# Kernel tuning notes

Measured on AMD Instinct MI355X. Metric: run time of the kernel, lower is better.

## Reference

```python
import jax, jax.numpy as jnp
import numpy as np

B, N, E, H, L, T, IN = 32, 512, 32768, 64, 2, 2, 8
TAU = 0.5


def setup_inputs() -> dict:
    key = jax.random.key(0)
    ks = jax.random.split(key, 32)
    f = lambda i, shape, s=0.05: jax.random.normal(ks[i], shape, jnp.float32) * s
    u = jax.random.uniform(ks[3], (B, E, T), jnp.float32, 1e-6, 1.0 - 1e-6)
    return {
        "inputs": f(0, (B, N, IN), 1.0),
        "hidden": f(1, (B, N, H), 1.0),
        "edge_logits": f(2, (B, E, T), 1.0),
        "gumbel": -jnp.log(-jnp.log(u)),  # standard Gumbel noise (deterministic here)
        "send_edges": jax.random.randint(ks[4], (E,), 0, N),
        "recv_edges": jax.random.randint(ks[5], (E,), 0, N),
        "W1": f(6, (L, T, H, 2 * H)), "b1": f(7, (L, T, H)),
        "W2": f(8, (L, T, H, H)), "b2": f(9, (L, T, H)),
        "Whr": f(10, (H, L * H)), "Whi": f(11, (H, L * H)), "Whh": f(12, (H, L * H)),
        "Wir": f(13, (H, IN)), "bir": f(14, (H,)),
        "Wii": f(15, (H, IN)), "bii": f(16, (H,)),
        "Win": f(17, (H, IN)), "bin_w": f(18, (H,)),
        "Wm1": f(19, (H, H)), "bm1": f(20, (H,)),
        "Wm2": f(21, (H, H)), "bm2": f(22, (H,)),
        "Wdf": f(23, (N, N * H), 0.005), "bdf": f(24, (N,)),
        "Wloc": f(25, (N, N * H), 0.005), "bloc": f(26, (N,)),
        "Wscale": f(27, (N, N * H), 0.005), "bscale": f(28, (N,)),
    }


def _lin(x, W, b):
    return jnp.einsum('...i,oi->...o', x, W) + b


def reference(inputs, hidden, edge_logits, gumbel, send_edges, recv_edges,
              W1, b1, W2, b2, Whr, Whi, Whh,
              Wir, bir, Wii, bii, Win, bin_w,
              Wm1, bm1, Wm2, bm2,
              Wdf, bdf, Wloc, bloc, Wscale, bscale):
    # hard gumbel-softmax (straight-through)
    y_soft = jax.nn.softmax((edge_logits + gumbel) / TAU, axis=-1)
    y_hard = jax.nn.one_hot(jnp.argmax(y_soft, axis=-1), T, dtype=y_soft.dtype)
    edges = jax.lax.stop_gradient(y_hard - y_soft) + y_soft  # [B,E,T]

    # normalized receiver degree (zeros -> 1), as in edge2node_mat / degree
    deg = jnp.zeros((N,), jnp.float32).at[recv_edges].add(1.0)
    deg = jnp.where(deg == 0, 1.0, deg)

    hidden_ = hidden
    aggs = []
    norm = float(T)  # skip_first_edge_type=False
    for k in range(L):
        pre = jnp.concatenate([hidden_[:, recv_edges], hidden_[:, send_edges]], axis=-1)  # [B,E,2H]
        all_msgs = jnp.zeros((B, E, H), pre.dtype)
        for t in range(T):  # per-edge-type tanh MLP (eval mode: dropout off)
            m = jnp.tanh(jnp.einsum('bef,hf->beh', pre, W1[k, t]) + b1[k, t])
            m = jnp.tanh(jnp.einsum('beh,gh->beg', m, W2[k, t]) + b2[k, t])
            all_msgs = all_msgs + m * edges[:, :, t:t + 1] / norm
        # scatter-mean onto receiver nodes (= normalized edge2node matmul)
        agg = jnp.zeros((B, N, H), all_msgs.dtype).at[:, recv_edges].add(all_msgs) / deg[None, :, None]
        hidden_ = agg
        aggs.append(agg)
    agg = jnp.concatenate(aggs, axis=-1)  # [B,N,L*H]

    r = jax.nn.sigmoid(_lin(inputs, Wir, bir) + jnp.einsum('bnf,of->bno', agg, Whr))
    i = jax.nn.sigmoid(_lin(inputs, Wii, bii) + jnp.einsum('bnf,of->bno', agg, Whi))
    n = jnp.tanh(_lin(inputs, Win, bin_w) + r * jnp.einsum('bnf,of->bno', agg, Whh))
    hidden_new = (1.0 - i) * n + i * hidden  # [B,N,H]

    pred = _lin(jax.nn.relu(_lin(hidden_new, Wm1, bm1)), Wm2, bm2)
    flat = pred.reshape(B, -1)  # [B, N*H]
    df = 2.0 + jax.nn.softplus(flat @ Wdf.T + bdf)      # StudentT domain maps
    loc = flat @ Wloc.T + bloc
    scale = jax.nn.softplus(flat @ Wscale.T + bscale)
    return df, loc, scale, hidden_new, edges
```

## Files before the change

### kernel.cpp

```cpp
#include <hip/hip_runtime.h>

#define B_  32
#define N_  512
#define E_  32768
#define H_  64
#define L_  2
#define T_  2
#define IN_ 8

typedef __attribute__((ext_vector_type(4))) float f32x4;
typedef __attribute__((ext_vector_type(8))) short bf16x8;
typedef __attribute__((ext_vector_type(4))) short s16x4;

__device__ __forceinline__ short f2bf(float f){
  unsigned u = __float_as_uint(f);
  u += 0x7FFFu + ((u >> 16) & 1u);
  return (short)(u >> 16);
}
__device__ __forceinline__ float bf2f(short s){
  return __uint_as_float(((unsigned)(unsigned short)s) << 16);
}
__device__ __forceinline__ bf16x8 pack8(f32x4 a, f32x4 b){
  bf16x8 r;
  r[0]=f2bf(a[0]); r[1]=f2bf(a[1]); r[2]=f2bf(a[2]); r[3]=f2bf(a[3]);
  r[4]=f2bf(b[0]); r[5]=f2bf(b[1]); r[6]=f2bf(b[2]); r[7]=f2bf(b[3]);
  return r;
}
__device__ __forceinline__ float fast_tanh(float x){
  float e = __expf(2.0f * x);
  return 1.0f - __fdividef(2.0f, e + 1.0f);
}
__device__ __forceinline__ float fast_sigm(float x){
  return __fdividef(1.0f, 1.0f + __expf(-x));
}
__device__ __forceinline__ float softplus_f(float x){
  return fmaxf(x, 0.0f) + log1pf(__expf(-fabsf(x)));
}

__global__ void k_edges(const float* __restrict__ logits, const float* __restrict__ gum,
                        float* __restrict__ edges_out, unsigned char* __restrict__ type_out){
  int i = blockIdx.x * 256 + threadIdx.x;
  if(i >= B_ * E_) return;
  float l0 = logits[2*i]   + gum[2*i];
  float l1 = logits[2*i+1] + gum[2*i+1];
  int t = (l1 > l0) ? 1 : 0;
  edges_out[2*i]   = t ? 0.f : 1.f;
  edges_out[2*i+1] = t ? 1.f : 0.f;
  type_out[i] = (unsigned char)t;
}

__global__ void k_hist(const int* __restrict__ recvE, int* __restrict__ hist){
  int e = blockIdx.x * 256 + threadIdx.x;
  if(e < E_) atomicAdd(&hist[recvE[e]], 1);
}
__global__ void k_scan(const int* __restrict__ hist, int* __restrict__ row_start,
                       float* __restrict__ deg){
  __shared__ int a[512], bbuf[512];
  int t = threadIdx.x;
  int h = hist[t];
  a[t] = h;
  __syncthreads();
  int* cur = a; int* nxt = bbuf;
  for(int off = 1; off < 512; off <<= 1){
    int v = cur[t] + (t >= off ? cur[t - off] : 0);
    nxt[t] = v;
    __syncthreads();
    int* tmp = cur; cur = nxt; nxt = tmp;
  }
  row_start[t] = cur[t] - h;
  if(t == 0) row_start[512] = E_;
  deg[t] = (h == 0) ? 1.0f : (float)h;
}

__global__ void k_hist2(const int* __restrict__ recvE, const unsigned char* __restrict__ typ,
                        int* __restrict__ n0){
  __shared__ int lh[512];
  int b = blockIdx.y, tid = threadIdx.x;
  lh[tid] = 0; lh[tid + 256] = 0;
  __syncthreads();
  int e0 = blockIdx.x * 2048;
  for(int k = 0; k < 8; ++k){
    int e = e0 + k*256 + tid;
    if(typ[(size_t)b*E_ + e] == 0) atomicAdd(&lh[recvE[e]], 1);
  }
  __syncthreads();
  if(lh[tid])       atomicAdd(&n0[b*512 + tid],       lh[tid]);
  if(lh[tid + 256]) atomicAdd(&n0[b*512 + tid + 256], lh[tid + 256]);
}
__global__ void k_scan2(const int* __restrict__ n0, const int* __restrict__ row_start,
                        int* __restrict__ stt){
  __shared__ int a[512], bbuf[512];
  __shared__ int tot;
  int b = blockIdx.x, t = threadIdx.x;
  int h = n0[b*512 + t];
  a[t] = h;
  __syncthreads();
  int* cur = a; int* nxt = bbuf;
  for(int off = 1; off < 512; off <<= 1){
    int v = cur[t] + (t >= off ? cur[t - off] : 0);
    nxt[t] = v;
    __syncthreads();
    int* tmp = cur; cur = nxt; nxt = tmp;
  }
  if(t == 511) tot = cur[511];
  __syncthreads();
  int excl = cur[t] - h;
  stt[(b*2    )*513 + t] = excl;
  stt[(b*2 + 1)*513 + t] = tot + row_start[t] - excl;
  if(t == 0){ stt[(b*2)*513 + 512] = tot; stt[(b*2+1)*513 + 512] = E_; }
}
__global__ void k_perm2(const int* __restrict__ recvE, const unsigned char* __restrict__ typ,
                        const int* __restrict__ stt, int* __restrict__ cur0,
                        int* __restrict__ cur1, unsigned short* __restrict__ perm2){
  int i = blockIdx.x * 256 + threadIdx.x;
  int b = i >> 15, e = i & (E_ - 1);
  int r = recvE[e];
  int pos;
  if(typ[i] == 0) pos = stt[(b*2  )*513 + r] + atomicAdd(&cur0[b*512 + r], 1);
  else            pos = stt[(b*2+1)*513 + r] + atomicAdd(&cur1[b*512 + r], 1);
  perm2[(size_t)b*E_ + pos] = (unsigned short)e;
}

__launch_bounds__(256, 2)
__global__ void k_prep(const float* __restrict__ hid,
                       const float* __restrict__ W1, const float* __restrict__ b1,
                       unsigned short* __restrict__ P, int layer){
  __shared__ __align__(16) short WT[256 * 64];
  __shared__ float bias[256];
  __shared__ float hidl[32 * 64];

  const int tid = threadIdx.x;
  const int b   = blockIdx.y;
  const int nbase = blockIdx.x * 32;
  const float* W1k = W1 + layer * (T_ * H_ * 2 * H_);

  {
    int col = tid, slot = col >> 6, h = col & 63;
    int t = slot & 1, prt = slot >> 1;
    const float* src = W1k + t*8192 + h*128 + prt*64;
#pragma unroll
    for(int u = 0; u < 8; ++u){
      bf16x8 v = pack8(*(const f32x4*)(src + u*8), *(const f32x4*)(src + u*8 + 4));
      int bo = col*128 + ((u*16) ^ ((col & 7) << 4));
      *(bf16x8*)((char*)WT + bo) = v;
    }
    bias[col] = (slot < 2) ? b1[layer*128 + t*64 + h] : 0.0f;
  }
  {
    const float* src = hid + ((size_t)b*N_ + nbase)*H_;
    ((f32x4*)hidl)[tid]       = ((const f32x4*)src)[tid];
    ((f32x4*)hidl)[tid + 256] = ((const f32x4*)src)[tid + 256];
  }
  __syncthreads();

  const int col = tid;
  for(int n = 0; n < 32; ++n){
    const float* hrow = hidl + n*64;
    float acc = bias[col];
#pragma unroll
    for(int u = 0; u < 8; ++u){
      int bo = col*128 + ((u*16) ^ ((col & 7) << 4));
      bf16x8 wv = *(const bf16x8*)((const char*)WT + bo);
#pragma unroll
      for(int i = 0; i < 8; ++i) acc += hrow[u*8 + i] * bf2f(wv[i]);
    }
    P[(((size_t)b*N_ + nbase + n) << 8) + col] = (unsigned short)f2bf(acc);
  }
}

__launch_bounds__(256, 6)
__global__ void k_msg(const unsigned short* __restrict__ P,
                      const float* __restrict__ W2, const float* __restrict__ b2,
                      const int* __restrict__ recvE, const int* __restrict__ sendE,
                      const unsigned short* __restrict__ perm2,
                      const int* __restrict__ stt, const float* __restrict__ deg,
                      float* __restrict__ agg, int layer){
  __shared__ __align__(16) short m1_lds[64 * 64];
  __shared__ float acc[8][64];
  __shared__ float b2_lds[128];
  __shared__ short rl_lds[64];

  const int tid  = threadIdx.x;
  const int w    = tid >> 6, lane = tid & 63;
  const int l15  = lane & 15, l4 = lane >> 4;
  const int b    = blockIdx.y;
  const int nodeBase = blockIdx.x * 8;

  const float* W2k = W2 + layer * (T_ * H_ * H_);

  if(tid < 128) b2_lds[tid] = b2[layer*128 + tid];
  acc[tid >> 6][tid & 63] = 0.0f;
  { int t2 = tid + 256; acc[t2 >> 6][t2 & 63] = 0.0f; }

  bf16x8 B2f[2][2];
#pragma unroll
  for(int t = 0; t < 2; ++t)
#pragma unroll
    for(int ks = 0; ks < 2; ++ks){
      const float* p = W2k + (t*64 + w*16 + l15)*64 + ks*32 + l4*8;
      B2f[t][ks] = pack8(*(const f32x4*)p, *(const f32x4*)(p+4));
    }

  const int gcol = w*16 + l15;
  const unsigned short* permB = perm2 + (size_t)b * E_;
  const int* sttB = stt + b*2*513;

#pragma unroll
  for(int seg = 0; seg < 2; ++seg){
    const int s0 = sttB[seg*513 + nodeBase];
    const int s1 = sttB[seg*513 + nodeBase + 8];
    const int ntiles = (s1 - s0 + 63) >> 6;
    for(int it = 0; it < ntiles; ++it){
      const int sbase = s0 + it*64;
      {
        int el = tid >> 2, part = tid & 3;
        int s = sbase + el;
        int h0 = part * 16;
        int bo0 = el*128 + ((h0*2)      ^ ((el & 7) << 4));
        int bo1 = el*128 + ((h0*2 + 16) ^ ((el & 7) << 4));
        if(s < s1){
          int eid = permB[s];
          int rv = recvE[eid], sd = sendE[eid];
          if(part == 0) rl_lds[el] = (short)(rv - nodeBase);
          const unsigned short* pr = P + (((size_t)b*N_ + rv) << 8) + seg*64 + h0;
          const unsigned short* ps = P + (((size_t)b*N_ + sd) << 8) + (2+seg)*64 + h0;
          bf16x8 r0 = *(const bf16x8*)pr,  r1 = *(const bf16x8*)(pr + 8);
          bf16x8 q0 = *(const bf16x8*)ps,  q1 = *(const bf16x8*)(ps + 8);
          bf16x8 o0, o1;
#pragma unroll
          for(int i = 0; i < 8; ++i){
            o0[i] = f2bf(fast_tanh(bf2f(r0[i]) + bf2f(q0[i])));
            o1[i] = f2bf(fast_tanh(bf2f(r1[i]) + bf2f(q1[i])));
          }
          *(bf16x8*)((char*)m1_lds + bo0) = o0;
          *(bf16x8*)((char*)m1_lds + bo1) = o1;
        }else{
          if(part == 0) rl_lds[el] = 255;
          bf16x8 z = {};
          *(bf16x8*)((char*)m1_lds + bo0) = z;
          *(bf16x8*)((char*)m1_lds + bo1) = z;
        }
      }
      __syncthreads();

      f32x4 C2[4];
      { float bv = b2_lds[seg*64 + gcol];
#pragma unroll
        for(int ef = 0; ef < 4; ++ef) C2[ef] = (f32x4){bv, bv, bv, bv}; }
#pragma unroll
      for(int ks = 0; ks < 2; ++ks){
#pragma unroll
        for(int ef = 0; ef < 4; ++ef){
          int e = ef*16 + l15;
          int byteoff = e*128 + (((ks*32 + l4*8)*2) ^ ((e & 7) << 4));
          bf16x8 A = *(const bf16x8*)((const char*)m1_lds + byteoff);
          C2[ef] = __builtin_amdgcn_mfma_f32_16x16x32_bf16(A, B2f[seg][ks], C2[ef], 0, 0, 0);
        }
      }
      {
        int prl = -1; float pend = 0.f;
#pragma unroll
        for(int ef = 0; ef < 4; ++ef){
          s16x4 rl4 = *(const s16x4*)&rl_lds[ef*16 + l4*4];
#pragma unroll
          for(int r = 0; r < 4; ++r){
            int rl = rl4[r];
            if(rl != prl){
              if(prl >= 0) atomicAdd(&acc[prl][gcol], pend);
              pend = 0.f;
              prl = (rl == 255) ? -1 : rl;
            }
            if(rl != 255) pend += fast_tanh(C2[ef][r]);
          }
        }
        if(prl >= 0) atomicAdd(&acc[prl][gcol], pend);
      }
      __syncthreads();
    }
  }

#pragma unroll
  for(int q = 0; q < 2; ++q){
    int idx = tid + q*256;
    int rl = idx >> 6, g = idx & 63;
    int node = nodeBase + rl;
    agg[(((size_t)b*N_ + node) << 6) + g] = acc[rl][g] * 0.5f / deg[node];
  }
}

__launch_bounds__(256, 2)
__global__ void k_gru(const float* __restrict__ x, const float* __restrict__ hid,
                      const float* __restrict__ agg0, const float* __restrict__ agg1,
                      const float* __restrict__ Whr, const float* __restrict__ Whi,
                      const float* __restrict__ Whh,
                      const float* __restrict__ Wir, const float* __restrict__ bir,
                      const float* __restrict__ Wii, const float* __restrict__ bii,
                      const float* __restrict__ Win, const float* __restrict__ binw,
                      float* __restrict__ hnew){
  __shared__ short WhrT[128*64], WhiT[128*64], WhhT[128*64];
  __shared__ float WxT[3][8*64];
  __shared__ float bias[3][64];
  __shared__ float agg_lds[4][128];

  int tid = threadIdx.x;
  for(int s = tid; s < 8192; s += 256){
    int g = s >> 7, f = s & 127;
    WhrT[f*64+g] = f2bf(Whr[s]);
    WhiT[f*64+g] = f2bf(Whi[s]);
    WhhT[f*64+g] = f2bf(Whh[s]);
  }
  for(int s = tid; s < 512; s += 256){
    int g = s >> 3, j = s & 7;
    WxT[0][j*64+g] = Wir[s]; WxT[1][j*64+g] = Wii[s]; WxT[2][j*64+g] = Win[s];
  }
  if(tid < 64){ bias[0][tid] = bir[tid]; bias[1][tid] = bii[tid]; bias[2][tid] = binw[tid]; }
  __syncthreads();

  int w = tid >> 6, lane = tid & 63;
  for(int j = 0; j < 8; ++j){
    int id = blockIdx.x*32 + j*4 + w;
    size_t base = (size_t)id * 64;
    agg_lds[w][lane]      = agg0[base + lane];
    agg_lds[w][64 + lane] = agg1[base + lane];

    float ar = bias[0][lane], ai = bias[1][lane], an = bias[2][lane], ah = 0.f;
    const float* xp = x + (size_t)id * 8;
#pragma unroll
    for(int jj = 0; jj < 8; ++jj){
      float xv = xp[jj];
      ar += xv * WxT[0][jj*64+lane];
      ai += xv * WxT[1][jj*64+lane];
      an += xv * WxT[2][jj*64+lane];
    }
#pragma unroll 4
    for(int f = 0; f < 128; ++f){
      float av = agg_lds[w][f];
      ar += av * bf2f(WhrT[f*64+lane]);
      ai += av * bf2f(WhiT[f*64+lane]);
      ah += av * bf2f(WhhT[f*64+lane]);
    }
    float r  = fast_sigm(ar);
    float ii = fast_sigm(ai);
    float ng = fast_tanh(an + r * ah);
    float ho = hid[base + lane];
    hnew[base + lane] = (1.0f - ii) * ng + ii * ho;
  }
}

__launch_bounds__(256, 2)
__global__ void k_pred(const float* __restrict__ hnew,
                       const float* __restrict__ Wm1, const float* __restrict__ bm1,
                       const float* __restrict__ Wm2, const float* __restrict__ bm2,
                       unsigned short* __restrict__ flatbf){
  __shared__ float W1T[64*64], W2T[64*64];
  __shared__ float bias1[64], bias2[64];
  __shared__ float h_lds[4][64], t_lds[4][64];
  int tid = threadIdx.x;
  for(int s = tid; s < 4096; s += 256){
    int g = s >> 6, h = s & 63;
    W1T[h*64+g] = Wm1[s];
    W2T[h*64+g] = Wm2[s];
  }
  if(tid < 64){ bias1[tid] = bm1[tid]; bias2[tid] = bm2[tid]; }
  __syncthreads();

  int w = tid >> 6, lane = tid & 63;
  for(int j = 0; j < 8; ++j){
    int id = blockIdx.x*32 + j*4 + w;
    size_t base = (size_t)id * 64;
    h_lds[w][lane] = hnew[base + lane];
    float a = bias1[lane];
#pragma unroll 4
    for(int h = 0; h < 64; ++h) a += h_lds[w][h] * W1T[h*64+lane];
    a = fmaxf(a, 0.0f);
    t_lds[w][lane] = a;
    float p = bias2[lane];
#pragma unroll 4
    for(int h = 0; h < 64; ++h) p += t_lds[w][h] * W2T[h*64+lane];
    flatbf[base + lane] = (unsigned short)f2bf(p);
  }
}

__launch_bounds__(256, 6)
__global__ void k_out(const float* __restrict__ Wdf, const float* __restrict__ Wloc,
                      const float* __restrict__ Wsc,
                      const unsigned short* __restrict__ flatbf,
                      float* __restrict__ pacc){
  const int bid = blockIdx.x;
  const int mt  = bid >> 5;
  const int kb  = bid & 31;
  const int row0 = mt * 32;
  const int mat  = row0 >> 9;
  const int rloc = row0 & 511;
  const float* W = (mat == 0) ? Wdf : (mat == 1) ? Wloc : Wsc;

  const int tid = threadIdx.x, w = tid >> 6, lane = tid & 63;
  const int l15 = lane & 15, l4 = lane >> 4;
  const float* wp = W + (size_t)(rloc + (w & 1)*16 + l15)*32768 + kb*1024 + l4*8;
  const unsigned short* fp = flatbf + (size_t)((w >> 1)*16 + l15)*32768 + kb*1024 + l4*8;

  f32x4 acc0 = {}, acc1 = {};
#pragma unroll 4
  for(int ks = 0; ks < 32; ks += 2){
    f32x4 a0 = *(const f32x4*)(wp + ks*32);
    f32x4 a1 = *(const f32x4*)(wp + ks*32 + 4);
    bf16x8 Bv0 = *(const bf16x8*)(fp + ks*32);
    f32x4 a2 = *(const f32x4*)(wp + ks*32 + 32);
    f32x4 a3 = *(const f32x4*)(wp + ks*32 + 36);
    bf16x8 Bv1 = *(const bf16x8*)(fp + ks*32 + 32);
    acc0 = __builtin_amdgcn_mfma_f32_16x16x32_bf16(pack8(a0, a1), Bv0, acc0, 0, 0, 0);
    acc1 = __builtin_amdgcn_mfma_f32_16x16x32_bf16(pack8(a2, a3), Bv1, acc1, 0, 0, 0);
  }
#pragma unroll
  for(int r = 0; r < 4; ++r){
    int grow = row0 + (w & 1)*16 + l4*4 + r;
    atomicAdd(&pacc[grow*32 + (w >> 1)*16 + l15], acc0[r] + acc1[r]);
  }
}

__global__ void k_fin(const float* __restrict__ pacc,
                      const float* __restrict__ bdf, const float* __restrict__ bloc,
                      const float* __restrict__ bsc, float* __restrict__ out){
  int i = blockIdx.x*256 + threadIdx.x;
  int mat = i >> 14;
  int rem = i & 16383;
  int b = rem >> 9, og = rem & 511;
  float s = pacc[(mat*512 + og)*32 + b];
  s += (mat == 0 ? bdf : mat == 1 ? bloc : bsc)[og];
  float res = (mat == 0) ? 2.0f + softplus_f(s) : (mat == 1) ? s : softplus_f(s);
  out[i] = res;
}

extern "C" void kernel_launch(void* const* d_in, const int* in_sizes, int n_in,
                              void* d_out, int out_size, void* d_ws, size_t ws_size,
                              hipStream_t stream){
  (void)in_sizes; (void)n_in; (void)out_size; (void)ws_size;
  const float* inputs = (const float*)d_in[0];
  const float* hidden = (const float*)d_in[1];
  const float* elog   = (const float*)d_in[2];
  const float* gum    = (const float*)d_in[3];
  const int*   sendE  = (const int*)  d_in[4];
  const int*   recvE  = (const int*)  d_in[5];
  const float* W1   = (const float*)d_in[6];
  const float* b1   = (const float*)d_in[7];
  const float* W2   = (const float*)d_in[8];
  const float* b2   = (const float*)d_in[9];
  const float* Whr  = (const float*)d_in[10];
  const float* Whi  = (const float*)d_in[11];
  const float* Whh  = (const float*)d_in[12];
  const float* Wir  = (const float*)d_in[13]; const float* bir  = (const float*)d_in[14];
  const float* Wii  = (const float*)d_in[15]; const float* bii  = (const float*)d_in[16];
  const float* Win  = (const float*)d_in[17]; const float* binw = (const float*)d_in[18];
  const float* Wm1  = (const float*)d_in[19]; const float* bm1  = (const float*)d_in[20];
  const float* Wm2  = (const float*)d_in[21]; const float* bm2  = (const float*)d_in[22];
  const float* Wdf  = (const float*)d_in[23]; const float* bdf  = (const float*)d_in[24];
  const float* Wloc = (const float*)d_in[25]; const float* bloc = (const float*)d_in[26];
  const float* Wsc  = (const float*)d_in[27]; const float* bsc  = (const float*)d_in[28];

  float* out       = (float*)d_out;
  float* out_hid   = out + 49152;
  float* out_edges = out + 1097728;

  char* ws = (char*)d_ws;
  float* agg0 = (float*)(ws);
  float* agg1 = (float*)(ws + 4194304);
  unsigned short* P = (unsigned short*)(ws + 8388608);
  unsigned short* flatbf = (unsigned short*)(ws + 8388608);
  unsigned short* perm2 = (unsigned short*)(ws + 16777216);
  unsigned char* typ = (unsigned char*)(ws + 18874368);
  int*   hist      = (int*)(ws + 19922944);
  int*   row_start = (int*)(ws + 19924992);
  float* deg       = (float*)(ws + 19929088);
  int*   n0        = (int*)(ws + 19931136);
  int*   cur0      = (int*)(ws + 19996672);
  int*   cur1      = (int*)(ws + 20062208);
  int*   stt       = (int*)(ws + 20127744);
  float* pacc      = agg0;

  hipMemsetAsync(hist, 0, 2048, stream);
  hipMemsetAsync(n0, 0, 3*65536, stream);

  k_edges<<<4096, 256, 0, stream>>>(elog, gum, out_edges, typ);
  k_hist<<<128, 256, 0, stream>>>(recvE, hist);
  k_scan<<<1, 512, 0, stream>>>(hist, row_start, deg);
  k_hist2<<<dim3(16, 32), 256, 0, stream>>>(recvE, typ, n0);
  k_scan2<<<32, 512, 0, stream>>>(n0, row_start, stt);
  k_perm2<<<4096, 256, 0, stream>>>(recvE, typ, stt, cur0, cur1, perm2);

  k_prep<<<dim3(16, 32), 256, 0, stream>>>(hidden, W1, b1, P, 0);
  k_msg<<<dim3(64, 32), 256, 0, stream>>>(P, W2, b2, recvE, sendE,
                                          perm2, stt, deg, agg0, 0);
  k_prep<<<dim3(16, 32), 256, 0, stream>>>(agg0, W1, b1, P, 1);
  k_msg<<<dim3(64, 32), 256, 0, stream>>>(P, W2, b2, recvE, sendE,
                                          perm2, stt, deg, agg1, 1);

  k_gru<<<512, 256, 0, stream>>>(inputs, hidden, agg0, agg1,
                                 Whr, Whi, Whh, Wir, bir, Wii, bii, Win, binw, out_hid);
  k_pred<<<512, 256, 0, stream>>>(out_hid, Wm1, bm1, Wm2, bm2, flatbf);
  hipMemsetAsync(pacc, 0, 1536*32*4, stream);
  k_out<<<1536, 256, 0, stream>>>(Wdf, Wloc, Wsc, flatbf, pacc);
  k_fin<<<192, 256, 0, stream>>>(pacc, bdf, bloc, bsc, out);
}
```

Measured before the change: 523.5 us.

## Software-pipeline edge gathers in k_msg with double-buffered LDS and faster tanh

Merges the two segment loops of the message kernel into one tile loop. It double-buffers the m1 and rl LDS tiles so only one barrier per tile is needed. The index chain (perm, then recv/send, then the P rows) is prefetched one to two tiles ahead so gather latency overlaps the MFMA and atomic work. It also switches tanh and sigmoid to exp2/rcp intrinsics and packs bf16 with v_cvt_pk_bf16_f32. The costs are more registers and LDS, which may lower occupancy under the launch bound of 6 blocks.

```diff
diff --git a/kernel.cpp b/kernel.cpp
--- a/kernel.cpp
+++ b/kernel.cpp
@@ -11,6 +11,7 @@
 typedef __attribute__((ext_vector_type(4))) float f32x4;
 typedef __attribute__((ext_vector_type(8))) short bf16x8;
 typedef __attribute__((ext_vector_type(4))) short s16x4;
+typedef __attribute__((ext_vector_type(4))) unsigned u32x4;
 
 __device__ __forceinline__ short f2bf(float f){
   unsigned u = __float_as_uint(f);
@@ -26,12 +27,21 @@
   r[4]=f2bf(b[0]); r[5]=f2bf(b[1]); r[6]=f2bf(b[2]); r[7]=f2bf(b[3]);
   return r;
 }
+__device__ __forceinline__ unsigned cvt_pk_bf16(float lo, float hi){
+  unsigned r;
+  asm("v_cvt_pk_bf16_f32 %0, %1, %2" : "=v"(r) : "v"(lo), "v"(hi));
+  return r;
+}
+__device__ __forceinline__ float lo16f(unsigned u){ return __uint_as_float(u << 16); }
+__device__ __forceinline__ float hi16f(unsigned u){ return __uint_as_float(u & 0xffff0000u); }
+
 __device__ __forceinline__ float fast_tanh(float x){
-  float e = __expf(2.0f * x);
-  return 1.0f - __fdividef(2.0f, e + 1.0f);
+  float e = __builtin_amdgcn_exp2f(x * 2.8853900817779268f);
+  float r = __builtin_amdgcn_rcpf(e + 1.0f);
+  return __builtin_fmaf(-2.0f, r, 1.0f);
 }
 __device__ __forceinline__ float fast_sigm(float x){
-  return __fdividef(1.0f, 1.0f + __expf(-x));
+  return __builtin_amdgcn_rcpf(1.0f + __builtin_amdgcn_exp2f(x * -1.4426950408889634f));
 }
 __device__ __forceinline__ float softplus_f(float x){
   return fmaxf(x, 0.0f) + log1pf(__expf(-fabsf(x)));
@@ -175,10 +185,10 @@
                       const unsigned short* __restrict__ perm2,
                       const int* __restrict__ stt, const float* __restrict__ deg,
                       float* __restrict__ agg, int layer){
-  __shared__ __align__(16) short m1_lds[64 * 64];
+  __shared__ __align__(16) short m1_lds[2][64 * 64];
   __shared__ float acc[8][64];
   __shared__ float b2_lds[128];
-  __shared__ short rl_lds[64];
+  __shared__ short rl_lds[2][64];
 
   const int tid  = threadIdx.x;
   const int w    = tid >> 6, lane = tid & 63;
@@ -204,80 +214,124 @@
   const int gcol = w*16 + l15;
   const unsigned short* permB = perm2 + (size_t)b * E_;
   const int* sttB = stt + b*2*513;
-
-#pragma unroll
-  for(int seg = 0; seg < 2; ++seg){
-    const int s0 = sttB[seg*513 + nodeBase];
-    const int s1 = sttB[seg*513 + nodeBase + 8];
-    const int ntiles = (s1 - s0 + 63) >> 6;
-    for(int it = 0; it < ntiles; ++it){
-      const int sbase = s0 + it*64;
-      {
-        int el = tid >> 2, part = tid & 3;
-        int s = sbase + el;
-        int h0 = part * 16;
-        int bo0 = el*128 + ((h0*2)      ^ ((el & 7) << 4));
-        int bo1 = el*128 + ((h0*2 + 16) ^ ((el & 7) << 4));
-        if(s < s1){
-          int eid = permB[s];
-          int rv = recvE[eid], sd = sendE[eid];
-          if(part == 0) rl_lds[el] = (short)(rv - nodeBase);
-          const unsigned short* pr = P + (((size_t)b*N_ + rv) << 8) + seg*64 + h0;
-          const unsigned short* ps = P + (((size_t)b*N_ + sd) << 8) + (2+seg)*64 + h0;
-          bf16x8 r0 = *(const bf16x8*)pr,  r1 = *(const bf16x8*)(pr + 8);
-          bf16x8 q0 = *(const bf16x8*)ps,  q1 = *(const bf16x8*)(ps + 8);
-          bf16x8 o0, o1;
-#pragma unroll
-          for(int i = 0; i < 8; ++i){
-            o0[i] = f2bf(fast_tanh(bf2f(r0[i]) + bf2f(q0[i])));
-            o1[i] = f2bf(fast_tanh(bf2f(r1[i]) + bf2f(q1[i])));
+  const int s0a = sttB[nodeBase],       s1a = sttB[nodeBase + 8];
+  const int s0b = sttB[513 + nodeBase], s1b = sttB[513 + nodeBase + 8];
+  const int nt0 = (s1a - s0a + 63) >> 6;
+  const int nt  = nt0 + ((s1b - s0b + 63) >> 6);
+
+  const int el = tid >> 2, part = tid & 3;
+  const int h0 = part * 16;
+  const int bo0 = el*128 + ((h0*2)      ^ ((el & 7) << 4));
+  const int bo1 = el*128 + ((h0*2 + 16) ^ ((el & 7) << 4));
+
+  auto SLIM = [&](int tt, int &s, int &lim){
+    if(tt < nt0){ s = s0a + tt*64 + el; lim = s1a; }
+    else        { s = s0b + (tt - nt0)*64 + el; lim = s1b; }
+  };
+
+  int pm = 0, rv = 0, sd = 0, rl_cur = 255;
+  bool v_cur = false;
+  u32x4 PR0 = {}, PR1 = {}, PS0 = {}, PS1 = {};
+
+  auto ISSUE_P = [&](int tt, int rvv, int sdv, bool v){
+    if(v){
+      int sg = (tt >= nt0);
+      const unsigned short* pr = P + (((size_t)b*N_ + rvv) << 8) + sg*64 + h0;
+      const unsigned short* ps = P + (((size_t)b*N_ + sdv) << 8) + (2 + sg)*64 + h0;
+      PR0 = *(const u32x4*)pr; PR1 = *(const u32x4*)(pr + 8);
+      PS0 = *(const u32x4*)ps; PS1 = *(const u32x4*)(ps + 8);
+    }else{
+      PR0 = (u32x4){}; PR1 = (u32x4){}; PS0 = (u32x4){}; PS1 = (u32x4){};
+    }
+  };
+
+  if(nt > 0){
+    int s, lim;
+    SLIM(0, s, lim); bool v0 = s < lim;
+    int e0 = v0 ? (int)permB[s] : 0;
+    int rv0 = v0 ? recvE[e0] : 0, sd0 = v0 ? sendE[e0] : 0;
+    rl_cur = v0 ? (rv0 - nodeBase) : 255; v_cur = v0;
+    ISSUE_P(0, rv0, sd0, v0);
+    SLIM(1, s, lim); bool v1 = s < lim;
+    int e1 = v1 ? (int)permB[s] : 0;
+    rv = v1 ? recvE[e1] : 0; sd = v1 ? sendE[e1] : 0;
+    SLIM(2, s, lim);
+    pm = (s < lim) ? (int)permB[s] : 0;
+  }
+
+  for(int ti = 0; ti < nt; ++ti){
+    const int c = ti & 1;
+    {
+      unsigned pk0[4], pk1[4];
+      if(v_cur){
+#pragma unroll
+        for(int j = 0; j < 4; ++j){
+          float a0 = lo16f(PR0[j]) + lo16f(PS0[j]);
+          float a1 = hi16f(PR0[j]) + hi16f(PS0[j]);
+          pk0[j] = cvt_pk_bf16(fast_tanh(a0), fast_tanh(a1));
+          float c0 = lo16f(PR1[j]) + lo16f(PS1[j]);
+          float c1 = hi16f(PR1[j]) + hi16f(PS1[j]);
+          pk1[j] = cvt_pk_bf16(fast_tanh(c0), fast_tanh(c1));
+        }
+      }else{
+#pragma unroll
+        for(int j = 0; j < 4; ++j){ pk0[j] = 0; pk1[j] = 0; }
+      }
+      u32x4 v0_ = { pk0[0], pk0[1], pk0[2], pk0[3] };
+      u32x4 v1_ = { pk1[0], pk1[1], pk1[2], pk1[3] };
+      *(u32x4*)((char*)m1_lds[c] + bo0) = v0_;
+      *(u32x4*)((char*)m1_lds[c] + bo1) = v1_;
+      if(part == 0) rl_lds[c][el] = (short)rl_cur;
+    }
+    __syncthreads();
+
+    {
+      int s, lim;
+      SLIM(ti + 1, s, lim); bool v1 = s < lim;
+      rl_cur = v1 ? (rv - nodeBase) : 255; v_cur = v1;
+      ISSUE_P(ti + 1, rv, sd, v1);
+      SLIM(ti + 2, s, lim); bool v2 = s < lim;
+      int e2 = pm;
+      rv = v2 ? recvE[e2] : 0; sd = v2 ? sendE[e2] : 0;
+      SLIM(ti + 3, s, lim);
+      pm = (s < lim) ? (int)permB[s] : 0;
+    }
+
+    const int sg = (ti >= nt0) ? 1 : 0;
+    f32x4 C2[4];
+    { float bv = b2_lds[sg*64 + gcol];
+#pragma unroll
+      for(int ef = 0; ef < 4; ++ef) C2[ef] = (f32x4){bv, bv, bv, bv}; }
+#pragma unroll
+    for(int ks = 0; ks < 2; ++ks){
+#pragma unroll
+      for(int ef = 0; ef < 4; ++ef){
+        int e = ef*16 + l15;
+        int byteoff = e*128 + (((ks*32 + l4*8)*2) ^ ((e & 7) << 4));
+        bf16x8 A = *(const bf16x8*)((const char*)m1_lds[c] + byteoff);
+        C2[ef] = __builtin_amdgcn_mfma_f32_16x16x32_bf16(A, B2f[sg][ks], C2[ef], 0, 0, 0);
+      }
+    }
+    {
+      int prl = -1; float pend = 0.f;
+#pragma unroll
+      for(int ef = 0; ef < 4; ++ef){
+        s16x4 rl4 = *(const s16x4*)&rl_lds[c][ef*16 + l4*4];
+#pragma unroll
+        for(int r = 0; r < 4; ++r){
+          int rl = rl4[r];
+          if(rl != prl){
+            if(prl >= 0) atomicAdd(&acc[prl][gcol], pend);
+            pend = 0.f;
+            prl = (rl == 255) ? -1 : rl;
           }
-          *(bf16x8*)((char*)m1_lds + bo0) = o0;
-          *(bf16x8*)((char*)m1_lds + bo1) = o1;
-        }else{
-          if(part == 0) rl_lds[el] = 255;
-          bf16x8 z = {};
-          *(bf16x8*)((char*)m1_lds + bo0) = z;
-          *(bf16x8*)((char*)m1_lds + bo1) = z;
+          if(rl != 255) pend += fast_tanh(C2[ef][r]);
         }
       }
-      __syncthreads();
-
-      f32x4 C2[4];
-      { float bv = b2_lds[seg*64 + gcol];
-#pragma unroll
-        for(int ef = 0; ef < 4; ++ef) C2[ef] = (f32x4){bv, bv, bv, bv}; }
-#pragma unroll
-      for(int ks = 0; ks < 2; ++ks){
-#pragma unroll
-        for(int ef = 0; ef < 4; ++ef){
-          int e = ef*16 + l15;
-          int byteoff = e*128 + (((ks*32 + l4*8)*2) ^ ((e & 7) << 4));
-          bf16x8 A = *(const bf16x8*)((const char*)m1_lds + byteoff);
-          C2[ef] = __builtin_amdgcn_mfma_f32_16x16x32_bf16(A, B2f[seg][ks], C2[ef], 0, 0, 0);
-        }
-      }
-      {
-        int prl = -1; float pend = 0.f;
-#pragma unroll
-        for(int ef = 0; ef < 4; ++ef){
-          s16x4 rl4 = *(const s16x4*)&rl_lds[ef*16 + l4*4];
-#pragma unroll
-          for(int r = 0; r < 4; ++r){
-            int rl = rl4[r];
-            if(rl != prl){
-              if(prl >= 0) atomicAdd(&acc[prl][gcol], pend);
-              pend = 0.f;
-              prl = (rl == 255) ? -1 : rl;
-            }
-            if(rl != 255) pend += fast_tanh(C2[ef][r]);
-          }
-        }
-        if(prl >= 0) atomicAdd(&acc[prl][gcol], pend);
-      }
-      __syncthreads();
-    }
-  }
+      if(prl >= 0) atomicAdd(&acc[prl][gcol], pend);
+    }
+  }
+  __syncthreads();
 
 #pragma unroll
   for(int q = 0; q < 2; ++q){
```

Measured after the change: 1.430 ms. 2.73x slower.
